# Kernel tuning notes

Hardware: AMD Instinct MI355X
Metric: run time of the kernel (lower is better)

## Reference

```python
import jax, jax.numpy as jnp
import numpy as np

WEIGHT = 10.0
# illegal[i, j] == True  iff transition (i -> j) is illegal; from {(0,2),(1,0),(2,0),(2,1)}
_ILLEGAL = np.zeros((3, 3), dtype=bool)
for _i, _j in [(0, 2), (1, 0), (2, 0), (2, 1)]:
    _ILLEGAL[_i, _j] = True


def setup_inputs() -> dict:
    key = jax.random.key(0)
    phase_logits = jax.random.normal(key, (2048, 8192, 3), dtype=jnp.float32)
    return {"phase_logits": phase_logits}


def reference(phase_logits):
    B, T, C = phase_logits.shape
    illegal = jnp.asarray(_ILLEGAL)
    pred = jnp.argmax(phase_logits, axis=-1)          # [B, T]
    pt = pred[:, :-1]                                  # phase at t     [B, T-1]
    pt1 = pred[:, 1:]                                  # phase at t+1   [B, T-1]
    mask = illegal[pt, pt1]                            # [B, T-1] bool
    # logit of the (argmax) illegal phase at t+1: phase_logits[b, t+1, pt1]
    gathered = jnp.take_along_axis(phase_logits[:, 1:, :], pt1[..., None], axis=-1)[..., 0]
    loss = jnp.sum(jnp.where(mask, gathered * gathered, jnp.zeros_like(gathered)))
    count = jnp.sum(mask.astype(phase_logits.dtype))
    return jnp.where(count > 0, WEIGHT * loss / count, jnp.zeros_like(loss))
```

## Files before the change

kernel.cpp:

```cpp
#include <hip/hip_runtime.h>


#define TLEN      8192
#define TMASK     8191u
#define NTHREADS  256
#define KCH       8
#define NBLK      8192

struct alignas(4) F3 { float a, b, c; };

__device__ __forceinline__ F3 load_f3(const float* __restrict__ p) {
    F3 v;
    __builtin_memcpy(&v, p, sizeof(F3));
    return v;
}

__device__ __forceinline__ int argmax3_pack(F3 v) {
    float bm = v.a; int bi = 0;
    if (v.b > bm) { bm = v.b; bi = 1; }
    if (v.c > bm) { bm = v.c; bi = 2; }
    return (__float_as_int(bm) & ~3) | bi;
}

__global__ __launch_bounds__(NTHREADS) void pcl_main(const float* __restrict__ x,
                                                     float* __restrict__ part_loss,
                                                     unsigned int* __restrict__ part_cnt,
                                                     unsigned int total) {
    const unsigned int gsz = NBLK * NTHREADS;
    const unsigned int gid = blockIdx.x * NTHREADS + threadIdx.x;
    const int lane = threadIdx.x & 63;

    F3 own[KCH];
    #pragma unroll
    for (int j = 0; j < KCH; ++j) {
        unsigned int c = gid + (unsigned int)j * gsz;
        own[j] = load_f3(x + (size_t)3 * c);
    }

    F3 nbv[KCH];
    if (lane == 63) {
        #pragma unroll
        for (int j = 0; j < KCH; ++j) {
            unsigned int s = gid + (unsigned int)j * gsz + 1u;
            if (s >= total) s = total - 1u;
            nbv[j] = load_f3(x + (size_t)3 * s);
        }
    }

    int pk[KCH];
    #pragma unroll
    for (int j = 0; j < KCH; ++j) pk[j] = argmax3_pack(own[j]);

    int fb[KCH] = {};
    if (lane == 63) {
        #pragma unroll
        for (int j = 0; j < KCH; ++j) fb[j] = argmax3_pack(nbv[j]);
    }

    float loss = 0.0f;
    unsigned int cnt = 0;
    #pragma unroll
    for (int j = 0; j < KCH; ++j) {
        unsigned int c = gid + (unsigned int)j * gsz;
        int npk = __shfl_down(pk[j], 1, 64);
        if (lane == 63) npk = fb[j];
        if ((c & TMASK) != TMASK) {
            int code = (pk[j] & 3) * 3 + (npk & 3);
            if ((0xCC >> code) & 1) {
                float nmx = __int_as_float(npk & ~3);
                loss = fmaf(nmx, nmx, loss);
                cnt++;
            }
        }
    }

    #pragma unroll
    for (int off = 32; off > 0; off >>= 1) {
        loss += __shfl_down(loss, off, 64);
        cnt  += __shfl_down(cnt,  off, 64);
    }

    __shared__ float        sl[4];
    __shared__ unsigned int sc[4];
    int wid = threadIdx.x >> 6;
    if (lane == 0) { sl[wid] = loss; sc[wid] = cnt; }
    __syncthreads();

    if (threadIdx.x == 0) {
        part_loss[blockIdx.x] = sl[0] + sl[1] + sl[2] + sl[3];
        part_cnt[blockIdx.x]  = sc[0] + sc[1] + sc[2] + sc[3];
    }
}

__global__ __launch_bounds__(NTHREADS) void pcl_final(const float* __restrict__ part_loss,
                                                      const unsigned int* __restrict__ part_cnt,
                                                      float* __restrict__ out, int npart) {
    double L = 0.0;
    unsigned int C = 0;
    for (int i = threadIdx.x; i < npart; i += NTHREADS) {
        L += (double)part_loss[i];
        C += part_cnt[i];
    }
    #pragma unroll
    for (int off = 32; off > 0; off >>= 1) {
        L += __shfl_down(L, off, 64);
        C += __shfl_down(C, off, 64);
    }
    __shared__ double       sl[4];
    __shared__ unsigned int sc[4];
    int lane = threadIdx.x & 63;
    int wid  = threadIdx.x >> 6;
    if (lane == 0) { sl[wid] = L; sc[wid] = C; }
    __syncthreads();
    if (threadIdx.x == 0) {
        double       Lt = sl[0] + sl[1] + sl[2] + sl[3];
        unsigned int Ct = sc[0] + sc[1] + sc[2] + sc[3];
        out[0] = (Ct > 0u) ? (float)(10.0 * Lt / (double)Ct) : 0.0f;
    }
}

extern "C" void kernel_launch(void* const* d_in, const int* in_sizes, int n_in,
                              void* d_out, int out_size, void* d_ws, size_t ws_size,
                              hipStream_t stream) {
    const float* x = (const float*)d_in[0];
    const unsigned int total = (unsigned int)(in_sizes[0] / 3);

    float*        part_loss = (float*)d_ws;
    unsigned int* part_cnt  = (unsigned int*)((char*)d_ws + (size_t)NBLK * sizeof(float));

    pcl_main<<<NBLK, NTHREADS, 0, stream>>>(x, part_loss, part_cnt, total);
    pcl_final<<<1, NTHREADS, 0, stream>>>(part_loss, part_cnt, (float*)d_out, NBLK);
}
```

Before: 276.4 us.

## Assign contiguous time slabs per block and share neighbor argmax via LDS

Result: no change. 274.7 us (-0.6%).

```diff
diff --git a/kernel.cpp b/kernel.cpp
--- a/kernel.cpp
+++ b/kernel.cpp
@@ -1,11 +1,10 @@
 #include <hip/hip_runtime.h>
 
 
+#define NTHREADS  256
+#define SLAB      2048
+#define JITER     8
 #define TLEN      8192
-#define TMASK     8191u
-#define NTHREADS  256
-#define KCH       8
-#define NBLK      8192
 
 struct alignas(4) F3 { float a, b, c; };
 
@@ -24,47 +23,45 @@
 
 __global__ __launch_bounds__(NTHREADS) void pcl_main(const float* __restrict__ x,
                                                      float* __restrict__ part_loss,
-                                                     unsigned int* __restrict__ part_cnt,
-                                                     unsigned int total) {
-    const unsigned int gsz = NBLK * NTHREADS;
-    const unsigned int gid = blockIdx.x * NTHREADS + threadIdx.x;
-    const int lane = threadIdx.x & 63;
+                                                     unsigned int* __restrict__ part_cnt) {
+    const int tid  = threadIdx.x;
+    const int lane = tid & 63;
+    const int wv   = tid >> 6;
+    const float* xb = x + (size_t)blockIdx.x * SLAB * 3;
 
-    F3 own[KCH];
+    F3 own[JITER];
     #pragma unroll
-    for (int j = 0; j < KCH; ++j) {
-        unsigned int c = gid + (unsigned int)j * gsz;
-        own[j] = load_f3(x + (size_t)3 * c);
+    for (int j = 0; j < JITER; ++j)
+        own[j] = load_f3(xb + (size_t)3 * (tid + j * NTHREADS));
+
+    const bool has_next = ((blockIdx.x & 3u) != 3u);
+    F3 nextv = own[0];
+    if (tid == NTHREADS - 1 && has_next)
+        nextv = load_f3(xb + (size_t)3 * SLAB);
+
+    int pk[JITER];
+    #pragma unroll
+    for (int j = 0; j < JITER; ++j) pk[j] = argmax3_pack(own[j]);
+
+    __shared__ int sm[4][JITER];
+    if (lane == 0) {
+        #pragma unroll
+        for (int j = 0; j < JITER; ++j) sm[wv][j] = pk[j];
     }
-
-    F3 nbv[KCH];
-    if (lane == 63) {
-        #pragma unroll
-        for (int j = 0; j < KCH; ++j) {
-            unsigned int s = gid + (unsigned int)j * gsz + 1u;
-            if (s >= total) s = total - 1u;
-            nbv[j] = load_f3(x + (size_t)3 * s);
-        }
-    }
-
-    int pk[KCH];
-    #pragma unroll
-    for (int j = 0; j < KCH; ++j) pk[j] = argmax3_pack(own[j]);
-
-    int fb[KCH] = {};
-    if (lane == 63) {
-        #pragma unroll
-        for (int j = 0; j < KCH; ++j) fb[j] = argmax3_pack(nbv[j]);
-    }
+    __syncthreads();
 
     float loss = 0.0f;
     unsigned int cnt = 0;
     #pragma unroll
-    for (int j = 0; j < KCH; ++j) {
-        unsigned int c = gid + (unsigned int)j * gsz;
+    for (int j = 0; j < JITER; ++j) {
         int npk = __shfl_down(pk[j], 1, 64);
-        if (lane == 63) npk = fb[j];
-        if ((c & TMASK) != TMASK) {
+        if (lane == 63) {
+            if (wv < 3)              npk = sm[wv + 1][j];
+            else if (j < JITER - 1)  npk = sm[0][j + 1];
+            else                     npk = argmax3_pack(nextv);
+        }
+        bool valid = !(wv == 3 && lane == 63 && j == JITER - 1 && !has_next);
+        if (valid) {
             int code = (pk[j] & 3) * 3 + (npk & 3);
             if ((0xCC >> code) & 1) {
                 float nmx = __int_as_float(npk & ~3);
@@ -82,11 +79,10 @@
 
     __shared__ float        sl[4];
     __shared__ unsigned int sc[4];
-    int wid = threadIdx.x >> 6;
-    if (lane == 0) { sl[wid] = loss; sc[wid] = cnt; }
+    if (lane == 0) { sl[wv] = loss; sc[wv] = cnt; }
     __syncthreads();
 
-    if (threadIdx.x == 0) {
+    if (tid == 0) {
         part_loss[blockIdx.x] = sl[0] + sl[1] + sl[2] + sl[3];
         part_cnt[blockIdx.x]  = sc[0] + sc[1] + sc[2] + sc[3];
     }
@@ -123,11 +119,12 @@
                               void* d_out, int out_size, void* d_ws, size_t ws_size,
                               hipStream_t stream) {
     const float* x = (const float*)d_in[0];
-    const unsigned int total = (unsigned int)(in_sizes[0] / 3);
+    const int B = in_sizes[0] / (3 * TLEN);
+    const int grid = B * (TLEN / SLAB);
 
     float*        part_loss = (float*)d_ws;
-    unsigned int* part_cnt  = (unsigned int*)((char*)d_ws + (size_t)NBLK * sizeof(float));
+    unsigned int* part_cnt  = (unsigned int*)((char*)d_ws + (size_t)grid * sizeof(float));
 
-    pcl_main<<<NBLK, NTHREADS, 0, stream>>>(x, part_loss, part_cnt, total);
-    pcl_final<<<1, NTHREADS, 0, stream>>>(part_loss, part_cnt, (float*)d_out, NBLK);
+    pcl_main<<<grid, NTHREADS, 0, stream>>>(x, part_loss, part_cnt);
+    pcl_final<<<1, NTHREADS, 0, stream>>>(part_loss, part_cnt, (float*)d_out, grid);
 }
```
